# Performance work log

Measured on AMD Instinct MI355X. Metric: run time of the kernel, lower is better.

Reference implementation:

```python
import jax, jax.numpy as jnp
import numpy as np

N_NODES = 100000
N_EDGES = 1280000
IN_DIM = 256
OUT_DIM = 64


def setup_inputs() -> dict:
    key = jax.random.key(0)
    k1, k2, k3, k4, k5, k6 = jax.random.split(key, 6)
    x = jax.random.normal(k1, (N_NODES, IN_DIM), dtype=jnp.float32)
    support_rows = jax.random.randint(k2, (N_EDGES,), 0, N_NODES, dtype=jnp.int64)
    support_cols = jax.random.randint(k3, (N_EDGES,), 0, N_NODES, dtype=jnp.int64)
    support_vals = jax.random.uniform(k4, (N_EDGES,), dtype=jnp.float32)
    weight = jax.random.normal(k5, (IN_DIM, OUT_DIM), dtype=jnp.float32) * 0.05
    bias = jax.random.normal(k6, (OUT_DIM,), dtype=jnp.float32) * 0.05
    return {
        "x": x,
        "support_rows": support_rows,
        "support_cols": support_cols,
        "support_vals": support_vals,
        "weight": weight,
        "bias": bias,
    }


def reference(x, support_rows, support_cols, support_vals, weight, bias):
    # dropout=0, training=False -> dropout is identity
    # pre_sup = X @ W : [N, out_dim]
    pre_sup = jnp.matmul(x, weight)
    # sparse support (COO) @ pre_sup : gather source rows, scale, scatter-add to dest rows
    gathered = pre_sup[support_cols] * support_vals[:, None]  # [E, out_dim]
    out = jax.ops.segment_sum(gathered, support_rows, num_segments=N_NODES)
    out = out + bias
    return jax.nn.relu(out)
```

## Files before the change

### kernel.cpp

```cpp
#include <hip/hip_runtime.h>
#include <hip/hip_bf16.h>
#include <stdint.h>

#define N_NODES 100000
#define N_EDGES 1280000
#define IN_DIM  256
#define OUT_DIM 64
#define NB1     98
#define GEMM_BLOCKS ((N_NODES + 63) / 64)
#define PART_SZ 12500

typedef __attribute__((ext_vector_type(8))) short bf16x8;
typedef __attribute__((ext_vector_type(4))) float f32x4;
typedef __attribute__((ext_vector_type(4))) unsigned short u16x4;

__device__ __forceinline__ unsigned short f32_to_bf16(float f) {
    union { float f; unsigned int u; } c; c.f = f;
    unsigned int u = c.u;
    u += 0x7fffu + ((u >> 16) & 1u);
    return (unsigned short)(u >> 16);
}
__device__ __forceinline__ float bf16_to_f32(unsigned short h) {
    union { unsigned int u; float f; } c; c.u = ((unsigned int)h) << 16; return c.f;
}

__global__ __launch_bounds__(256) void wpack_zero_kernel(const float* __restrict__ w,
                                                         unsigned short* __restrict__ wbf,
                                                         int* __restrict__ deg) {
    const int tid = threadIdx.x;
    const int base = blockIdx.x * 1024 + tid * 4;
    #pragma unroll
    for (int q = 0; q < 4; ++q) {
        const int i = base + q;
        if (i < N_NODES) deg[i] = 0;
    }
    if (blockIdx.x == 0) {
        for (int i = tid; i < IN_DIM * OUT_DIM; i += 256) {
            const int k = i >> 6, n = i & 63;
            const int kt = k >> 5, q = (k >> 3) & 3, j = k & 7;
            const int t = n >> 4, l = n & 15;
            wbf[((kt * 4 + t) * 64 + q * 16 + l) * 8 + j] = f32_to_bf16(w[i]);
        }
    }
}

__global__ __launch_bounds__(256, 4) void gemm_hist_kernel(const float* __restrict__ x,
                                                           const unsigned short* __restrict__ wbf,
                                                           unsigned short* __restrict__ pre,
                                                           const int* __restrict__ rows,
                                                           int* __restrict__ deg) {
    __shared__ __align__(16) unsigned short wt[IN_DIM * OUT_DIM];

    const int tid = threadIdx.x;
    const int wave = tid >> 6;
    const int lane = tid & 63;
    const int ln16 = lane & 15;
    const int quad = lane >> 4;

    const int R0 = blockIdx.x * 64;
    const int arow = R0 + wave * 16 + ln16;
    const float* xrow = x + (size_t)(arow < N_NODES ? arow : N_NODES - 1) * IN_DIM + quad * 8;

    f32x4 xa[8], xb[8];
    #pragma unroll
    for (int kt = 0; kt < 8; ++kt) {
        xa[kt] = *(const f32x4*)(xrow + kt * 32);
        xb[kt] = *(const f32x4*)(xrow + kt * 32 + 4);
    }

    #pragma unroll
    for (int i = 0; i < 8; ++i)
        *(bf16x8*)&wt[i * 2048 + tid * 8] = *(const bf16x8*)(wbf + i * 2048 + tid * 8);

    __syncthreads();

    f32x4 acc[4] = {};

    #pragma unroll
    for (int kt = 0; kt < 8; ++kt) {
        bf16x8 a;
        a[0] = (short)f32_to_bf16(xa[kt].x); a[1] = (short)f32_to_bf16(xa[kt].y);
        a[2] = (short)f32_to_bf16(xa[kt].z); a[3] = (short)f32_to_bf16(xa[kt].w);
        a[4] = (short)f32_to_bf16(xb[kt].x); a[5] = (short)f32_to_bf16(xb[kt].y);
        a[6] = (short)f32_to_bf16(xb[kt].z); a[7] = (short)f32_to_bf16(xb[kt].w);
        #pragma unroll
        for (int t = 0; t < 4; ++t) {
            bf16x8 b = *(const bf16x8*)&wt[((kt * 4 + t) * 64 + lane) * 8];
            acc[t] = __builtin_amdgcn_mfma_f32_16x16x32_bf16(a, b, acc[t], 0, 0, 0);
        }
    }

    const int rbase = R0 + wave * 16 + quad * 4;
    #pragma unroll
    for (int t = 0; t < 4; ++t) {
        #pragma unroll
        for (int r = 0; r < 4; ++r) {
            const int rr = rbase + r;
            if (rr < N_NODES)
                pre[(size_t)rr * OUT_DIM + t * 16 + ln16] = f32_to_bf16(acc[t][r]);
        }
    }

    for (int e = blockIdx.x * 256 + tid; e < N_EDGES; e += GEMM_BLOCKS * 256) {
        atomicAdd(&deg[rows[e]], 1);
    }
}

__global__ __launch_bounds__(256) void scan1_kernel(const int* __restrict__ deg,
                                                    int* __restrict__ off,
                                                    int* __restrict__ bsum) {
    __shared__ int s[256];
    const int t = threadIdx.x;
    const int base = blockIdx.x * 1024 + t * 4;
    int d[4];
    #pragma unroll
    for (int q = 0; q < 4; ++q) {
        const int i = base + q;
        d[q] = i < N_NODES ? deg[i] : 0;
    }
    const int tsum = d[0] + d[1] + d[2] + d[3];
    s[t] = tsum;
    __syncthreads();
    #pragma unroll
    for (int o = 1; o < 256; o <<= 1) {
        const int add = t >= o ? s[t - o] : 0;
        __syncthreads();
        s[t] += add;
        __syncthreads();
    }
    int run = t > 0 ? s[t - 1] : 0;
    #pragma unroll
    for (int q = 0; q < 4; ++q) {
        const int i = base + q;
        if (i < N_NODES) off[i] = run;
        run += d[q];
    }
    if (t == 255) bsum[blockIdx.x] = run;
}

__global__ __launch_bounds__(128) void scan2_kernel(const int* __restrict__ bsum,
                                                    int* __restrict__ boff,
                                                    int* __restrict__ off) {
    __shared__ int s[128];
    const int t = threadIdx.x;
    const int v = t < NB1 ? bsum[t] : 0;
    s[t] = v;
    __syncthreads();
    #pragma unroll
    for (int o = 1; o < 128; o <<= 1) {
        const int add = t >= o ? s[t - o] : 0;
        __syncthreads();
        s[t] += add;
        __syncthreads();
    }
    if (t < NB1) boff[t] = t > 0 ? s[t - 1] : 0;
    if (t == 127) off[N_NODES] = s[127];
}

__global__ __launch_bounds__(256) void scan3_kernel(int* __restrict__ off,
                                                    const int* __restrict__ boff,
                                                    int* __restrict__ cursor) {
    const int i = blockIdx.x * 256 + threadIdx.x;
    if (i < N_NODES) {
        const int v = off[i] + boff[i >> 10];
        off[i] = v;
        cursor[i] = v;
    }
}

__global__ __launch_bounds__(256) void reorder_kernel(const int* __restrict__ rows,
                                                      const int* __restrict__ cols,
                                                      const float* __restrict__ vals,
                                                      int* __restrict__ cursor,
                                                      unsigned long long* __restrict__ epack) {
    const int part = blockIdx.x & 7;
    const int lo = part * PART_SZ;
    const int hi = lo + PART_SZ;
    const int base = (blockIdx.x >> 3) * 2048 + threadIdx.x;
    #pragma unroll
    for (int k = 0; k < 8; ++k) {
        const int e = base + k * 256;
        const int r = rows[e];
        if (r >= lo && r < hi) {
            const int c = cols[e];
            const float v = vals[e];
            const int slot = atomicAdd(&cursor[r], 1);
            epack[slot] = ((unsigned long long)__float_as_uint(v) << 32) | (unsigned int)c;
        }
    }
}

__global__ __launch_bounds__(256) void gather_kernel(const int* __restrict__ off,
                                                     const unsigned long long* __restrict__ epack,
                                                     const unsigned short* __restrict__ pre,
                                                     const float* __restrict__ bias,
                                                     float* __restrict__ out) {
    const int v = blockIdx.x * 4 + (threadIdx.x >> 6);
    const int j = threadIdx.x & 63;
    if (v >= N_NODES) return;
    const int s = off[v];
    const int e = off[v + 1];
    float acc = 0.0f;
    int i = s;
    for (; i + 4 <= e; i += 4) {
        unsigned long long ee[4];
        float p[4];
        #pragma unroll
        for (int q = 0; q < 4; ++q) ee[q] = epack[i + q];
        #pragma unroll
        for (int q = 0; q < 4; ++q)
            p[q] = bf16_to_f32(pre[(size_t)(unsigned int)(ee[q] & 0xffffffffu) * OUT_DIM + j]);
        #pragma unroll
        for (int q = 0; q < 4; ++q)
            acc = fmaf(p[q], __uint_as_float((unsigned int)(ee[q] >> 32)), acc);
    }
    for (; i < e; ++i) {
        const unsigned long long e0 = epack[i];
        acc = fmaf(bf16_to_f32(pre[(size_t)(unsigned int)(e0 & 0xffffffffu) * OUT_DIM + j]),
                   __uint_as_float((unsigned int)(e0 >> 32)), acc);
    }
    const float r = acc + bias[j];
    out[(size_t)v * OUT_DIM + j] = r > 0.0f ? r : 0.0f;
}

extern "C" void kernel_launch(void* const* d_in, const int* in_sizes, int n_in,
                              void* d_out, int out_size, void* d_ws, size_t ws_size,
                              hipStream_t stream) {
    const float* x    = (const float*)d_in[0];
    const int* rows   = (const int*)d_in[1];
    const int* cols   = (const int*)d_in[2];
    const float* vals = (const float*)d_in[3];
    const float* w    = (const float*)d_in[4];
    const float* bias = (const float*)d_in[5];
    float* out        = (float*)d_out;

    unsigned short* pre = (unsigned short*)d_ws;
    int* deg    = (int*)(pre + (size_t)N_NODES * OUT_DIM);
    int* off    = deg + N_NODES;
    int* cursor = off + N_NODES + 4;
    int* bsum   = cursor + N_NODES;
    int* boff   = bsum + 128;
    unsigned long long* epack = (unsigned long long*)(boff + 128);

    unsigned short* wbf = (unsigned short*)cursor;

    wpack_zero_kernel<<<NB1, 256, 0, stream>>>(w, wbf, deg);

    gemm_hist_kernel<<<GEMM_BLOCKS, 256, 0, stream>>>(x, wbf, pre, rows, deg);

    scan1_kernel<<<NB1, 256, 0, stream>>>(deg, off, bsum);
    scan2_kernel<<<1, 128, 0, stream>>>(bsum, boff, off);
    scan3_kernel<<<(N_NODES + 255) / 256, 256, 0, stream>>>(off, boff, cursor);

    reorder_kernel<<<5000, 256, 0, stream>>>(rows, cols, vals, cursor, epack);

    gather_kernel<<<(N_NODES + 3) / 4, 256, 0, stream>>>(off, epack, pre, bias, out);
}
```

Baseline: 338.3 us.

## Split degree histogram into LDS-binned kernel and persist GEMM with prefetch

The global-atomic degree count is moved out of the GEMM into a separate kernel. It builds per-chunk histograms in shared memory over node slices and writes 16 partial arrays, which scan1 then sums. The GEMM becomes persistent with 521 blocks, each looping over tiles and prefetching the next tile's x rows into registers while the current one finishes. This cuts global atomic contention and launch-per-tile overhead. In exchange it adds an extra kernel, re-reads the rows array 7 times, and makes scan1 read 16 partial arrays.

```diff
diff --git a/kernel.cpp b/kernel.cpp
--- a/kernel.cpp
+++ b/kernel.cpp
@@ -7,12 +7,17 @@
 #define IN_DIM  256
 #define OUT_DIM 64
 #define NB1     98
-#define GEMM_BLOCKS ((N_NODES + 63) / 64)
+#define NTILES  ((N_NODES + 63) / 64)
+#define GB      521
 #define PART_SZ 12500
+
+#define HS    7
+#define HBINS 16000
+#define HC    16
+#define EPC   (N_EDGES / HC)
 
 typedef __attribute__((ext_vector_type(8))) short bf16x8;
 typedef __attribute__((ext_vector_type(4))) float f32x4;
-typedef __attribute__((ext_vector_type(4))) unsigned short u16x4;
 
 __device__ __forceinline__ unsigned short f32_to_bf16(float f) {
     union { float f; unsigned int u; } c; c.f = f;
@@ -24,31 +29,50 @@
     union { unsigned int u; float f; } c; c.u = ((unsigned int)h) << 16; return c.f;
 }
 
-__global__ __launch_bounds__(256) void wpack_zero_kernel(const float* __restrict__ w,
-                                                         unsigned short* __restrict__ wbf,
-                                                         int* __restrict__ deg) {
-    const int tid = threadIdx.x;
-    const int base = blockIdx.x * 1024 + tid * 4;
-    #pragma unroll
-    for (int q = 0; q < 4; ++q) {
-        const int i = base + q;
-        if (i < N_NODES) deg[i] = 0;
-    }
-    if (blockIdx.x == 0) {
-        for (int i = tid; i < IN_DIM * OUT_DIM; i += 256) {
-            const int k = i >> 6, n = i & 63;
-            const int kt = k >> 5, q = (k >> 3) & 3, j = k & 7;
-            const int t = n >> 4, l = n & 15;
-            wbf[((kt * 4 + t) * 64 + q * 16 + l) * 8 + j] = f32_to_bf16(w[i]);
-        }
-    }
-}
-
-__global__ __launch_bounds__(256, 4) void gemm_hist_kernel(const float* __restrict__ x,
-                                                           const unsigned short* __restrict__ wbf,
-                                                           unsigned short* __restrict__ pre,
-                                                           const int* __restrict__ rows,
-                                                           int* __restrict__ deg) {
+__global__ __launch_bounds__(256) void wpack_kernel(const float* __restrict__ w,
+                                                    unsigned short* __restrict__ wbf) {
+    for (int i = threadIdx.x; i < IN_DIM * OUT_DIM; i += 256) {
+        const int k = i >> 6, n = i & 63;
+        const int kt = k >> 5, q = (k >> 3) & 3, j = k & 7;
+        const int t = n >> 4, l = n & 15;
+        wbf[((kt * 4 + t) * 64 + q * 16 + l) * 8 + j] = f32_to_bf16(w[i]);
+    }
+}
+
+__global__ __launch_bounds__(256) void hist_kernel(const int* __restrict__ rows,
+                                                   int* __restrict__ partial) {
+    __shared__ int lh[HBINS];
+    const int s = blockIdx.x % HS;
+    const int c = blockIdx.x / HS;
+    const int lo = s * HBINS;
+    const int ncnt = (lo + HBINS <= N_NODES) ? HBINS : (N_NODES - lo);
+    for (int i = threadIdx.x; i < ncnt; i += 256) lh[i] = 0;
+    __syncthreads();
+    const int e1 = (c + 1) * EPC;
+    for (int e = c * EPC + threadIdx.x; e < e1; e += 256) {
+        const unsigned d = (unsigned)(rows[e] - lo);
+        if (d < (unsigned)ncnt) atomicAdd(&lh[d], 1);
+    }
+    __syncthreads();
+    int* dst = partial + (size_t)c * N_NODES + lo;
+    for (int i = threadIdx.x; i < ncnt; i += 256) dst[i] = lh[i];
+}
+
+__device__ __forceinline__ void issue_tile(const float* __restrict__ x, int tile,
+                                           int wave, int ln16, int quad,
+                                           f32x4 (&xa)[8], f32x4 (&xb)[8]) {
+    int arow = tile * 64 + wave * 16 + ln16;
+    const float* xrow = x + (size_t)(arow < N_NODES ? arow : N_NODES - 1) * IN_DIM + quad * 8;
+    #pragma unroll
+    for (int kt = 0; kt < 8; ++kt) {
+        xa[kt] = *(const f32x4*)(xrow + kt * 32);
+        xb[kt] = *(const f32x4*)(xrow + kt * 32 + 4);
+    }
+}
+
+__global__ __launch_bounds__(256, 4) void gemm_kernel(const float* __restrict__ x,
+                                                      const unsigned short* __restrict__ wbf,
+                                                      unsigned short* __restrict__ pre) {
     __shared__ __align__(16) unsigned short wt[IN_DIM * OUT_DIM];
 
     const int tid = threadIdx.x;
@@ -57,16 +81,8 @@
     const int ln16 = lane & 15;
     const int quad = lane >> 4;
 
-    const int R0 = blockIdx.x * 64;
-    const int arow = R0 + wave * 16 + ln16;
-    const float* xrow = x + (size_t)(arow < N_NODES ? arow : N_NODES - 1) * IN_DIM + quad * 8;
-
     f32x4 xa[8], xb[8];
-    #pragma unroll
-    for (int kt = 0; kt < 8; ++kt) {
-        xa[kt] = *(const f32x4*)(xrow + kt * 32);
-        xb[kt] = *(const f32x4*)(xrow + kt * 32 + 4);
-    }
+    issue_tile(x, blockIdx.x, wave, ln16, quad, xa, xb);
 
     #pragma unroll
     for (int i = 0; i < 8; ++i)
@@ -74,49 +90,54 @@
 
     __syncthreads();
 
-    f32x4 acc[4] = {};
-
-    #pragma unroll
-    for (int kt = 0; kt < 8; ++kt) {
-        bf16x8 a;
-        a[0] = (short)f32_to_bf16(xa[kt].x); a[1] = (short)f32_to_bf16(xa[kt].y);
-        a[2] = (short)f32_to_bf16(xa[kt].z); a[3] = (short)f32_to_bf16(xa[kt].w);
-        a[4] = (short)f32_to_bf16(xb[kt].x); a[5] = (short)f32_to_bf16(xb[kt].y);
-        a[6] = (short)f32_to_bf16(xb[kt].z); a[7] = (short)f32_to_bf16(xb[kt].w);
-        #pragma unroll
-        for (int t = 0; t < 4; ++t) {
-            bf16x8 b = *(const bf16x8*)&wt[((kt * 4 + t) * 64 + lane) * 8];
-            acc[t] = __builtin_amdgcn_mfma_f32_16x16x32_bf16(a, b, acc[t], 0, 0, 0);
-        }
-    }
-
-    const int rbase = R0 + wave * 16 + quad * 4;
-    #pragma unroll
-    for (int t = 0; t < 4; ++t) {
-        #pragma unroll
-        for (int r = 0; r < 4; ++r) {
-            const int rr = rbase + r;
-            if (rr < N_NODES)
-                pre[(size_t)rr * OUT_DIM + t * 16 + ln16] = f32_to_bf16(acc[t][r]);
-        }
-    }
-
-    for (int e = blockIdx.x * 256 + tid; e < N_EDGES; e += GEMM_BLOCKS * 256) {
-        atomicAdd(&deg[rows[e]], 1);
-    }
-}
-
-__global__ __launch_bounds__(256) void scan1_kernel(const int* __restrict__ deg,
+    #pragma clang loop unroll(disable)
+    for (int t = blockIdx.x; t < NTILES; t += GB) {
+        f32x4 acc[4] = {};
+        #pragma unroll
+        for (int kt = 0; kt < 8; ++kt) {
+            bf16x8 a;
+            a[0] = (short)f32_to_bf16(xa[kt].x); a[1] = (short)f32_to_bf16(xa[kt].y);
+            a[2] = (short)f32_to_bf16(xa[kt].z); a[3] = (short)f32_to_bf16(xa[kt].w);
+            a[4] = (short)f32_to_bf16(xb[kt].x); a[5] = (short)f32_to_bf16(xb[kt].y);
+            a[6] = (short)f32_to_bf16(xb[kt].z); a[7] = (short)f32_to_bf16(xb[kt].w);
+            #pragma unroll
+            for (int tt = 0; tt < 4; ++tt) {
+                bf16x8 b = *(const bf16x8*)&wt[((kt * 4 + tt) * 64 + lane) * 8];
+                acc[tt] = __builtin_amdgcn_mfma_f32_16x16x32_bf16(a, b, acc[tt], 0, 0, 0);
+            }
+        }
+
+        const int rbase = t * 64 + wave * 16 + quad * 4;
+        #pragma unroll
+        for (int tt = 0; tt < 4; ++tt) {
+            #pragma unroll
+            for (int r = 0; r < 4; ++r) {
+                const int rr = rbase + r;
+                if (rr < N_NODES)
+                    pre[(size_t)rr * OUT_DIM + tt * 16 + ln16] = f32_to_bf16(acc[tt][r]);
+            }
+        }
+
+        if (t + GB < NTILES)
+            issue_tile(x, t + GB, wave, ln16, quad, xa, xb);
+    }
+}
+
+__global__ __launch_bounds__(256) void scan1_kernel(const int* __restrict__ partial,
                                                     int* __restrict__ off,
                                                     int* __restrict__ bsum) {
     __shared__ int s[256];
     const int t = threadIdx.x;
     const int base = blockIdx.x * 1024 + t * 4;
-    int d[4];
-    #pragma unroll
-    for (int q = 0; q < 4; ++q) {
-        const int i = base + q;
-        d[q] = i < N_NODES ? deg[i] : 0;
+    int d[4] = {0, 0, 0, 0};
+    #pragma unroll
+    for (int c = 0; c < HC; ++c) {
+        const int* p = partial + (size_t)c * N_NODES;
+        #pragma unroll
+        for (int q = 0; q < 4; ++q) {
+            const int i = base + q;
+            if (i < N_NODES) d[q] += p[i];
+        }
     }
     const int tsum = d[0] + d[1] + d[2] + d[3];
     s[t] = tsum;
@@ -235,20 +256,22 @@
     float* out        = (float*)d_out;
 
     unsigned short* pre = (unsigned short*)d_ws;
-    int* deg    = (int*)(pre + (size_t)N_NODES * OUT_DIM);
-    int* off    = deg + N_NODES;
+    int* off    = (int*)(pre + (size_t)N_NODES * OUT_DIM);
     int* cursor = off + N_NODES + 4;
     int* bsum   = cursor + N_NODES;
     int* boff   = bsum + 128;
     unsigned long long* epack = (unsigned long long*)(boff + 128);
 
+    int* partial = (int*)epack;
     unsigned short* wbf = (unsigned short*)cursor;
 
-    wpack_zero_kernel<<<NB1, 256, 0, stream>>>(w, wbf, deg);
-
-    gemm_hist_kernel<<<GEMM_BLOCKS, 256, 0, stream>>>(x, wbf, pre, rows, deg);
-
-    scan1_kernel<<<NB1, 256, 0, stream>>>(deg, off, bsum);
+    wpack_kernel<<<1, 256, 0, stream>>>(w, wbf);
+
+    hist_kernel<<<HS * HC, 256, 0, stream>>>(rows, partial);
+
+    gemm_kernel<<<GB, 256, 0, stream>>>(x, wbf, pre);
+
+    scan1_kernel<<<NB1, 256, 0, stream>>>(partial, off, bsum);
     scan2_kernel<<<1, 128, 0, stream>>>(bsum, boff, off);
     scan3_kernel<<<(N_NODES + 255) / 256, 256, 0, stream>>>(off, boff, cursor);
 
```

Result: slower. 480.8 us (+42.1%).

## Replace global atomic degree histogram with LDS-privatized partial histograms

Applied to the files above, without the earlier changes.

Removes the global atomicAdd degree count that ran at the end of the GEMM kernel. A separate hist_kernel now builds per-chunk histograms in shared memory: 50 edge chunks times 4 node slices, with 16-bit counts packed two per word. scan1 then sums the 50 partials while it computes the offsets. This avoids contended global atomics, at the cost of reading the row indices four times, writing and re-reading about 10 MB of partials, and adding a kernel launch.

```diff
diff --git a/kernel.cpp b/kernel.cpp
--- a/kernel.cpp
+++ b/kernel.cpp
@@ -10,6 +10,11 @@
 #define GEMM_BLOCKS ((N_NODES + 63) / 64)
 #define PART_SZ 12500
 
+#define HSL   4
+#define HSB   25000
+#define HCH   50
+#define HEPC  (N_EDGES / HCH)
+
 typedef __attribute__((ext_vector_type(8))) short bf16x8;
 typedef __attribute__((ext_vector_type(4))) float f32x4;
 typedef __attribute__((ext_vector_type(4))) unsigned short u16x4;
@@ -24,31 +29,45 @@
     union { unsigned int u; float f; } c; c.u = ((unsigned int)h) << 16; return c.f;
 }
 
-__global__ __launch_bounds__(256) void wpack_zero_kernel(const float* __restrict__ w,
-                                                         unsigned short* __restrict__ wbf,
-                                                         int* __restrict__ deg) {
-    const int tid = threadIdx.x;
-    const int base = blockIdx.x * 1024 + tid * 4;
-    #pragma unroll
-    for (int q = 0; q < 4; ++q) {
-        const int i = base + q;
-        if (i < N_NODES) deg[i] = 0;
-    }
-    if (blockIdx.x == 0) {
-        for (int i = tid; i < IN_DIM * OUT_DIM; i += 256) {
-            const int k = i >> 6, n = i & 63;
-            const int kt = k >> 5, q = (k >> 3) & 3, j = k & 7;
-            const int t = n >> 4, l = n & 15;
-            wbf[((kt * 4 + t) * 64 + q * 16 + l) * 8 + j] = f32_to_bf16(w[i]);
-        }
-    }
-}
-
-__global__ __launch_bounds__(256, 4) void gemm_hist_kernel(const float* __restrict__ x,
-                                                           const unsigned short* __restrict__ wbf,
-                                                           unsigned short* __restrict__ pre,
-                                                           const int* __restrict__ rows,
-                                                           int* __restrict__ deg) {
+__global__ __launch_bounds__(256) void wpack_kernel(const float* __restrict__ w,
+                                                    unsigned short* __restrict__ wbf) {
+    const int i0 = blockIdx.x * 1024;
+    for (int i = i0 + threadIdx.x; i < i0 + 1024; i += 256) {
+        const int k = i >> 6, n = i & 63;
+        const int kt = k >> 5, q = (k >> 3) & 3, j = k & 7;
+        const int t = n >> 4, l = n & 15;
+        wbf[((kt * 4 + t) * 64 + q * 16 + l) * 8 + j] = f32_to_bf16(w[i]);
+    }
+}
+
+__global__ __launch_bounds__(256) void hist_kernel(const int* __restrict__ rows,
+                                                   unsigned short* __restrict__ partial) {
+    __shared__ unsigned int lh[HSB / 2];
+    const int s = blockIdx.x & 3;
+    const int c = blockIdx.x >> 2;
+    const int lo = s * HSB;
+    for (int i = threadIdx.x; i < HSB / 2; i += 256) lh[i] = 0u;
+    __syncthreads();
+    const int4* rp = (const int4*)(rows + c * HEPC);
+    for (int i = threadIdx.x; i < HEPC / 4; i += 256) {
+        const int4 r4 = rp[i];
+        const unsigned d0 = (unsigned)(r4.x - lo);
+        const unsigned d1 = (unsigned)(r4.y - lo);
+        const unsigned d2 = (unsigned)(r4.z - lo);
+        const unsigned d3 = (unsigned)(r4.w - lo);
+        if (d0 < HSB) atomicAdd(&lh[d0 >> 1], 1u << ((d0 & 1) * 16));
+        if (d1 < HSB) atomicAdd(&lh[d1 >> 1], 1u << ((d1 & 1) * 16));
+        if (d2 < HSB) atomicAdd(&lh[d2 >> 1], 1u << ((d2 & 1) * 16));
+        if (d3 < HSB) atomicAdd(&lh[d3 >> 1], 1u << ((d3 & 1) * 16));
+    }
+    __syncthreads();
+    unsigned int* dst = (unsigned int*)(partial + (size_t)c * N_NODES + lo);
+    for (int i = threadIdx.x; i < HSB / 2; i += 256) dst[i] = lh[i];
+}
+
+__global__ __launch_bounds__(256, 4) void gemm_kernel(const float* __restrict__ x,
+                                                      const unsigned short* __restrict__ wbf,
+                                                      unsigned short* __restrict__ pre) {
     __shared__ __align__(16) unsigned short wt[IN_DIM * OUT_DIM];
 
     const int tid = threadIdx.x;
@@ -100,24 +119,22 @@
                 pre[(size_t)rr * OUT_DIM + t * 16 + ln16] = f32_to_bf16(acc[t][r]);
         }
     }
-
-    for (int e = blockIdx.x * 256 + tid; e < N_EDGES; e += GEMM_BLOCKS * 256) {
-        atomicAdd(&deg[rows[e]], 1);
-    }
-}
-
-__global__ __launch_bounds__(256) void scan1_kernel(const int* __restrict__ deg,
+}
+
+__global__ __launch_bounds__(256) void scan1_kernel(const unsigned short* __restrict__ partial,
                                                     int* __restrict__ off,
                                                     int* __restrict__ bsum) {
     __shared__ int s[256];
     const int t = threadIdx.x;
     const int base = blockIdx.x * 1024 + t * 4;
-    int d[4];
-    #pragma unroll
-    for (int q = 0; q < 4; ++q) {
-        const int i = base + q;
-        d[q] = i < N_NODES ? deg[i] : 0;
-    }
+    int d[4] = {0, 0, 0, 0};
+    for (int c = 0; c < HCH; ++c) {
+        const u16x4 v = *(const u16x4*)(partial + (size_t)c * N_NODES + base);
+        d[0] += v[0]; d[1] += v[1]; d[2] += v[2]; d[3] += v[3];
+    }
+    #pragma unroll
+    for (int q = 0; q < 4; ++q)
+        if (base + q >= N_NODES) d[q] = 0;
     const int tsum = d[0] + d[1] + d[2] + d[3];
     s[t] = tsum;
     __syncthreads();
@@ -235,20 +252,22 @@
     float* out        = (float*)d_out;
 
     unsigned short* pre = (unsigned short*)d_ws;
-    int* deg    = (int*)(pre + (size_t)N_NODES * OUT_DIM);
-    int* off    = deg + N_NODES;
+    int* off    = (int*)(pre + (size_t)N_NODES * OUT_DIM);
     int* cursor = off + N_NODES + 4;
     int* bsum   = cursor + N_NODES;
     int* boff   = bsum + 128;
     unsigned long long* epack = (unsigned long long*)(boff + 128);
 
+    unsigned short* partial = (unsigned short*)epack;
     unsigned short* wbf = (unsigned short*)cursor;
 
-    wpack_zero_kernel<<<NB1, 256, 0, stream>>>(w, wbf, deg);
-
-    gemm_hist_kernel<<<GEMM_BLOCKS, 256, 0, stream>>>(x, wbf, pre, rows, deg);
-
-    scan1_kernel<<<NB1, 256, 0, stream>>>(deg, off, bsum);
+    wpack_kernel<<<16, 256, 0, stream>>>(w, wbf);
+
+    hist_kernel<<<HSL * HCH, 256, 0, stream>>>(rows, partial);
+
+    gemm_kernel<<<GEMM_BLOCKS, 256, 0, stream>>>(x, wbf, pre);
+
+    scan1_kernel<<<NB1, 256, 0, stream>>>(partial, off, bsum);
     scan2_kernel<<<1, 128, 0, stream>>>(bsum, boff, off);
     scan3_kernel<<<(N_NODES + 255) / 256, 256, 0, stream>>>(off, boff, cursor);
 
```

Measured after the change: 322.7 us. -4.6%, faster.
